# Kernel tuning notes

Measured on AMD Instinct MI355X. Metric: run time of the kernel, lower is better.

Reference implementation:

```python
import jax, jax.numpy as jnp
import numpy as np

LR = 0.1  # forward default lr; noise_std=0.0 default so no Langevin noise
B, DX, DY, H, K = 65536, 256, 64, 512, 4


def setup_inputs() -> dict:
    key = jax.random.key(0)
    ks = jax.random.split(key, 8)
    x = jax.random.normal(ks[0], (B, DX), dtype=jnp.float32)
    t = jax.random.randint(ks[1], (B,), 0, K, dtype=jnp.int64)
    # MLP params, Kaiming-ish scaling
    s1 = 1.0 / np.sqrt(DX + DY)
    s2 = 1.0 / np.sqrt(H)
    W1 = jax.random.normal(ks[2], (DX + DY, H), dtype=jnp.float32) * s1
    b1 = jnp.zeros((H,), jnp.float32)
    W2 = jax.random.normal(ks[3], (H, H), dtype=jnp.float32) * s2
    b2 = jnp.zeros((H,), jnp.float32)
    W3 = jax.random.normal(ks[4], (H, K), dtype=jnp.float32) * s2
    b3 = jnp.zeros((K,), jnp.float32)
    return {"x": x, "t": t, "W1": W1, "b1": b1, "W2": W2, "b2": b2,
            "W3": W3, "b3": b3, "steps": 20}


def reference(x, t, W1, b1, W2, b2, W3, b3, steps):
    # gather index: t.clamp_min(0) -> [B, 1]
    tc = jnp.clip(t, 0, None).astype(jnp.int32)[:, None]
    d_y = W1.shape[0] - x.shape[1]

    def energy_sum(y):
        h = jax.nn.relu(jnp.concatenate([x, y], axis=-1) @ W1 + b1)
        h = jax.nn.relu(h @ W2 + b2)
        e = h @ W3 + b3                      # [B, K]
        return jnp.take_along_axis(e, tc, axis=1).sum()

    grad_e = jax.grad(energy_sum)

    def step(y, _):
        return y - LR * grad_e(y), None

    y0 = jnp.zeros((x.shape[0], d_y), dtype=x.dtype)
    y_final, _ = jax.lax.scan(step, y0, None, length=steps)
    return y_final
```

## Files before the change

### kernel.cpp

```cpp
#include <hip/hip_runtime.h>

typedef _Float16 f16x8 __attribute__((ext_vector_type(8)));
typedef float f32x4 __attribute__((ext_vector_type(4)));

#define HID   512
#define DXD   256
#define DYD   64
#define NROWS 64
#define NTHR  1024
#define LRC   0.1f
#define TAU1  1e-4f
#define TAU2  1e-4f
#define SC12  2.44140625e-4f

#define OFF_W1YB 0
#define OFF_W1Y4 32768
#define OFF_W2B  65536
#define OFF_W2B3 327680
#define PH       589824
#define RB       1179648
#define OFF_RW1YB 0
#define OFF_RW2B  32768
#define RPA      294912
#define NCONV    884736

#define L_H0  0
#define L_H1  65536
#define HPL   65536
#define L_Y0  131072
#define L_Y1  139264
#define YPL   8192
#define L_TL  147456
#define SMEM_BYTES 147712

__device__ __forceinline__ void f2h2(float v, unsigned short* ph, unsigned short* pm) {
    unsigned short hb, mb;
    if (fabsf(v) >= 6.103515625e-05f) {
        _Float16 h = (_Float16)v;
        _Float16 m = (_Float16)((v - (float)h) * 4096.0f);
        hb = __builtin_bit_cast(unsigned short, h);
        mb = __builtin_bit_cast(unsigned short, m);
    } else {
        _Float16 m = (_Float16)(v * 4096.0f);
        hb = 0;
        mb = __builtin_bit_cast(unsigned short, m);
    }
    *ph = hb; *pm = mb;
}

template<int KSTEPS, int SROWA, int APL_>
__device__ __forceinline__ void gemmh1(const char* ldsA, const unsigned short* Bfrag,
                                       int l4, int l16, int lane, int ct,
                                       f32x4 acc[4], f32x4 accm[4])
{
    const int cb0 = l4 * 16;
    #pragma unroll
    for (int kk = 0; kk < KSTEPS; ++kk) {
        const int cb = kk * 64 + cb0;
        f16x8 ah[4], am[4];
        #pragma unroll
        for (int mt = 0; mt < 4; ++mt) {
            const int row = mt * 16 + l16;
            const int off = row * SROWA + (cb ^ ((row & 7) << 4));
            ah[mt] = *(const f16x8*)(ldsA + off);
            am[mt] = *(const f16x8*)(ldsA + APL_ + off);
        }
        const size_t boff = ((size_t)(ct * KSTEPS + kk) * 64 + lane) * 16;
        f16x8 bh = *(const f16x8*)((const char*)Bfrag + boff);
        f16x8 bm = *(const f16x8*)((const char*)(Bfrag + PH) + boff);
        #pragma unroll
        for (int mt = 0; mt < 4; ++mt) {
            acc[mt]  = __builtin_amdgcn_mfma_f32_16x16x32_f16(ah[mt], bh, acc[mt],  0, 0, 0);
            accm[mt] = __builtin_amdgcn_mfma_f32_16x16x32_f16(ah[mt], bm, accm[mt], 0, 0, 0);
            accm[mt] = __builtin_amdgcn_mfma_f32_16x16x32_f16(am[mt], bh, accm[mt], 0, 0, 0);
        }
    }
}

__device__ __attribute__((noinline))
float rescue_s2(const char* smem, int row, int col, float b2n,
                const unsigned short* __restrict__ wsb) {
    float r = b2n;
    const int xr = (row & 7) << 4;
    const int rb = row * 1024;
    const char* wh = (const char*)(wsb + RB + OFF_RW2B) + (size_t)col * 1024;
    const char* wm = (const char*)(wsb + RB + RPA + OFF_RW2B) + (size_t)col * 1024;
    for (int j0 = 0; j0 < HID; j0 += 8) {
        const int off = rb + ((j0 * 2) ^ xr);
        f16x8 h  = *(const f16x8*)(smem + L_H0 + off);
        f16x8 m_ = *(const f16x8*)(smem + L_H1 + off);
        f16x8 bh = *(const f16x8*)(wh + j0 * 2);
        f16x8 bm = *(const f16x8*)(wm + j0 * 2);
        #pragma unroll
        for (int u = 0; u < 8; ++u) {
            float hv = (float)h[u]  + (float)m_[u] * SC12;
            float wv = (float)bh[u] + (float)bm[u] * SC12;
            r = fmaf(hv, wv, r);
        }
    }
    return r;
}

__device__ __attribute__((noinline))
float rescue_s1(const char* smem, int row, int col, float cval,
                const unsigned short* __restrict__ wsb) {
    float r = cval;
    const int xr = (row & 7) << 4;
    const int rb = row * 128;
    const char* wh = (const char*)(wsb + RB + OFF_RW1YB) + (size_t)col * 128;
    const char* wm = (const char*)(wsb + RB + RPA + OFF_RW1YB) + (size_t)col * 128;
    for (int j0 = 0; j0 < DYD; j0 += 8) {
        const int off = rb + ((j0 * 2) ^ xr);
        f16x8 h  = *(const f16x8*)(smem + L_Y0 + off);
        f16x8 m_ = *(const f16x8*)(smem + L_Y1 + off);
        f16x8 bh = *(const f16x8*)(wh + j0 * 2);
        f16x8 bm = *(const f16x8*)(wm + j0 * 2);
        #pragma unroll
        for (int u = 0; u < 8; ++u) {
            float yv = (float)h[u]  + (float)m_[u] * SC12;
            float wv = (float)bh[u] + (float)bm[u] * SC12;
            r = fmaf(yv, wv, r);
        }
    }
    return r;
}

__global__ void wconv(const float* __restrict__ W1, const float* __restrict__ W2,
                      unsigned short* __restrict__ wsb)
{
    int i = blockIdx.x * blockDim.x + threadIdx.x;
    if (i >= NCONV) return;
    if (i < PH) {
        int il, KK, region;
        if (i < OFF_W1Y4)      { il = i;            KK = 2;  region = 0; }
        else if (i < OFF_W2B)  { il = i - OFF_W1Y4; KK = 16; region = 1; }
        else if (i < OFF_W2B3) { il = i - OFF_W2B;  KK = 16; region = 2; }
        else                   { il = i - OFF_W2B3; KK = 16; region = 3; }
        const int e    = il & 7;
        const int lane = (il >> 3) & 63;
        const int l16  = lane & 15;
        const int l4   = lane >> 4;
        const int rest = il >> 9;
        const int kk   = rest % KK;
        const int t    = rest / KK;
        const int n    = t * 16 + l16;
        const int k    = kk * 32 + l4 * 8 + e;
        float v;
        if (region == 0)      v = W1[(size_t)(256 + k) * 512 + n];
        else if (region == 1) v = W1[(size_t)(256 + n) * 512 + k];
        else if (region == 2) v = W2[(size_t)k * 512 + n];
        else                  v = W2[(size_t)n * 512 + k];
        f2h2(v, &wsb[i], &wsb[i + PH]);
    } else {
        int j = i - PH;
        float v;
        if (j < OFF_RW2B) { int n = j >> 6, k = j & 63;  v = W1[(size_t)(256 + k) * 512 + n]; }
        else { int jl = j - OFF_RW2B; int n = jl >> 9, k = jl & 511; v = W2[(size_t)k * 512 + n]; }
        f2h2(v, &wsb[RB + j], &wsb[RB + RPA + j]);
    }
}

__global__ __attribute__((amdgpu_flat_work_group_size(NTHR, NTHR), amdgpu_waves_per_eu(4, 4)))
void ebm_mfma(const float* __restrict__ x, const int* __restrict__ tt,
              const float* __restrict__ W1, const float* __restrict__ b1,
              const float* __restrict__ W2, const float* __restrict__ b2,
              const float* __restrict__ W3, const int* __restrict__ stepsp,
              const unsigned short* __restrict__ wsb, float* __restrict__ out)
{
    __shared__ __align__(16) char smem[SMEM_BYTES];

    const int tid  = threadIdx.x;
    const int w    = tid >> 6, lane = tid & 63;
    const int l4   = lane >> 4, l16 = lane & 15;
    const int r0   = blockIdx.x * NROWS;
    const int nt0  = w * 2;
    const int nsteps = *stepsp;

    if (tid < NROWS) {
        int tv = tt[r0 + tid];
        ((int*)(smem + L_TL))[tid] = tv < 0 ? 0 : tv;
    }
    for (int i = tid; i < 2 * YPL / 4; i += NTHR) ((unsigned*)(smem + L_Y0))[i] = 0u;

    {
        const float4* xg = (const float4*)(x + (size_t)r0 * DXD);
        #pragma unroll
        for (int j = 0; j < 4; ++j) {
            int i4 = j * NTHR + tid;
            ((float4*)(smem + L_H0))[i4] = xg[i4];
        }
    }
    __syncthreads();

    f32x4 c_reg[4][2];
    {
        float bb[2];
        #pragma unroll
        for (int nq = 0; nq < 2; ++nq) bb[nq] = b1[(nt0 + nq) * 16 + l16];
        #pragma unroll
        for (int mt = 0; mt < 4; ++mt)
            #pragma unroll
            for (int nq = 0; nq < 2; ++nq)
                c_reg[mt][nq] = (f32x4){bb[nq], bb[nq], bb[nq], bb[nq]};
        for (int i = 0; i < DXD; i += 4) {
            float wv[4][2];
            #pragma unroll
            for (int d = 0; d < 4; ++d)
                #pragma unroll
                for (int nq = 0; nq < 2; ++nq)
                    wv[d][nq] = W1[(size_t)(i + d) * HID + (nt0 + nq) * 16 + l16];
            #pragma unroll
            for (int mt = 0; mt < 4; ++mt)
                #pragma unroll
                for (int q = 0; q < 4; ++q) {
                    const int row = mt * 16 + l4 * 4 + q;
                    float4 xv = *(const float4*)(smem + L_H0 + row * 1024 + i * 4);
                    #pragma unroll
                    for (int nq = 0; nq < 2; ++nq) {
                        c_reg[mt][nq][q] = fmaf(xv.x, wv[0][nq], c_reg[mt][nq][q]);
                        c_reg[mt][nq][q] = fmaf(xv.y, wv[1][nq], c_reg[mt][nq][q]);
                        c_reg[mt][nq][q] = fmaf(xv.z, wv[2][nq], c_reg[mt][nq][q]);
                        c_reg[mt][nq][q] = fmaf(xv.w, wv[3][nq], c_reg[mt][nq][q]);
                    }
                }
        }
    }

    float b2v[2];
    #pragma unroll
    for (int nq = 0; nq < 2; ++nq) b2v[nq] = b2[(nt0 + nq) * 16 + l16];

    const int mt4 = w >> 2;
    const int nt4 = w & 3;
    f32x4 ym = (f32x4){0.f, 0.f, 0.f, 0.f};

    for (int s = 0; s < nsteps; ++s) {
        __syncthreads();

        unsigned mk = 0u;
        #pragma unroll
        for (int nq = 0; nq < 2; ++nq) {
            f32x4 acc[4], accm[4];
            #pragma unroll
            for (int mt = 0; mt < 4; ++mt) { acc[mt] = c_reg[mt][nq]; accm[mt] = (f32x4){0.f,0.f,0.f,0.f}; }
            gemmh1<2, 128, YPL>(smem + L_Y0, wsb + OFF_W1YB, l4, l16, lane, nt0 + nq, acc, accm);
            const int col = (nt0 + nq) * 16 + l16;
            unsigned tie = 0u;
            #pragma unroll
            for (int mt = 0; mt < 4; ++mt) {
                #pragma unroll
                for (int q = 0; q < 4; ++q) {
                    const int row = mt * 16 + l4 * 4 + q;
                    float v = acc[mt][q] + accm[mt][q] * SC12;
                    if (fabsf(v) < TAU1) tie |= 1u << (mt * 4 + q);
                    const int off = row * 1024 + ((col * 2) ^ ((row & 7) << 4));
                    if (v > 0.f) {
                        mk |= 1u << ((mt * 2 + nq) * 4 + q);
                        f2h2(v, (unsigned short*)(smem + L_H0 + off), (unsigned short*)(smem + L_H1 + off));
                    } else {
                        *(unsigned short*)(smem + L_H0 + off) = 0;
                        *(unsigned short*)(smem + L_H1 + off) = 0;
                    }
                }
            }
            if (__builtin_expect(tie != 0u, 0)) {
                #pragma unroll
                for (int mt = 0; mt < 4; ++mt) {
                    #pragma unroll
                    for (int q = 0; q < 4; ++q) {
                        if ((tie >> (mt * 4 + q)) & 1u) {
                            const int row = mt * 16 + l4 * 4 + q;
                            const float vr = rescue_s1(smem, row, col, c_reg[mt][nq][q], wsb);
                            const int off = row * 1024 + ((col * 2) ^ ((row & 7) << 4));
                            const unsigned bit = 1u << ((mt * 2 + nq) * 4 + q);
                            if (vr > 0.f) {
                                mk |= bit;
                                f2h2(vr, (unsigned short*)(smem + L_H0 + off), (unsigned short*)(smem + L_H1 + off));
                            } else {
                                mk &= ~bit;
                                *(unsigned short*)(smem + L_H0 + off) = 0;
                                *(unsigned short*)(smem + L_H1 + off) = 0;
                            }
                        }
                    }
                }
            }
            __builtin_amdgcn_sched_barrier(0);
        }
        __syncthreads();

        unsigned pos2 = 0u;
        #pragma unroll
        for (int nq = 0; nq < 2; ++nq) {
            f32x4 acc[4], accm[4];
            #pragma unroll
            for (int mt = 0; mt < 4; ++mt) { acc[mt] = (f32x4){b2v[nq],b2v[nq],b2v[nq],b2v[nq]}; accm[mt] = (f32x4){0.f,0.f,0.f,0.f}; }
            gemmh1<16, 1024, HPL>(smem + L_H0, wsb + OFF_W2B, l4, l16, lane, nt0 + nq, acc, accm);
            const int col = (nt0 + nq) * 16 + l16;
            unsigned tie = 0u;
            #pragma unroll
            for (int mt = 0; mt < 4; ++mt) {
                #pragma unroll
                for (int q = 0; q < 4; ++q) {
                    float v = acc[mt][q] + accm[mt][q] * SC12;
                    if (fabsf(v) < TAU2) tie |= 1u << (mt * 4 + q);
                    if (v > 0.f) pos2 |= 1u << ((mt * 2 + nq) * 4 + q);
                }
            }
            if (__builtin_expect(tie != 0u, 0)) {
                #pragma unroll
                for (int mt = 0; mt < 4; ++mt) {
                    #pragma unroll
                    for (int q = 0; q < 4; ++q) {
                        if ((tie >> (mt * 4 + q)) & 1u) {
                            const int row = mt * 16 + l4 * 4 + q;
                            const float vr = rescue_s2(smem, row, col, b2v[nq], wsb);
                            const unsigned bit = 1u << ((mt * 2 + nq) * 4 + q);
                            if (vr > 0.f) pos2 |= bit; else pos2 &= ~bit;
                        }
                    }
                }
            }
            __builtin_amdgcn_sched_barrier(0);
        }
        __syncthreads();

        #pragma unroll
        for (int mt = 0; mt < 4; ++mt) {
            #pragma unroll
            for (int nq = 0; nq < 2; ++nq) {
                const int col = (nt0 + nq) * 16 + l16;
                #pragma unroll
                for (int q = 0; q < 4; ++q) {
                    const int row = mt * 16 + l4 * 4 + q;
                    const int tv = ((const int*)(smem + L_TL))[row];
                    const int off = row * 1024 + ((col * 2) ^ ((row & 7) << 4));
                    if ((pos2 >> ((mt * 2 + nq) * 4 + q)) & 1u) {
                        f2h2(W3[col * 4 + tv],
                             (unsigned short*)(smem + L_H0 + off),
                             (unsigned short*)(smem + L_H1 + off));
                    } else {
                        *(unsigned short*)(smem + L_H0 + off) = 0;
                        *(unsigned short*)(smem + L_H1 + off) = 0;
                    }
                }
            }
        }
        __syncthreads();

        f32x4 g2vA[4], g2vB[4];
        {
            f32x4 acc[4], accm[4];
            #pragma unroll
            for (int mt = 0; mt < 4; ++mt) { acc[mt] = (f32x4){0.f,0.f,0.f,0.f}; accm[mt] = (f32x4){0.f,0.f,0.f,0.f}; }
            gemmh1<16, 1024, HPL>(smem + L_H0, wsb + OFF_W2B3, l4, l16, lane, nt0 + 0, acc, accm);
            #pragma unroll
            for (int mt = 0; mt < 4; ++mt)
                #pragma unroll
                for (int q = 0; q < 4; ++q)
                    g2vA[mt][q] = acc[mt][q] + accm[mt][q] * SC12;
        }
        __builtin_amdgcn_sched_barrier(0);
        {
            f32x4 acc[4], accm[4];
            #pragma unroll
            for (int mt = 0; mt < 4; ++mt) { acc[mt] = (f32x4){0.f,0.f,0.f,0.f}; accm[mt] = (f32x4){0.f,0.f,0.f,0.f}; }
            gemmh1<16, 1024, HPL>(smem + L_H0, wsb + OFF_W2B3, l4, l16, lane, nt0 + 1, acc, accm);
            #pragma unroll
            for (int mt = 0; mt < 4; ++mt)
                #pragma unroll
                for (int q = 0; q < 4; ++q)
                    g2vB[mt][q] = acc[mt][q] + accm[mt][q] * SC12;
        }
        __syncthreads();

        #pragma unroll
        for (int mt = 0; mt < 4; ++mt) {
            {
                const int col2 = ((nt0 + 0) * 16 + l16) * 2;
                #pragma unroll
                for (int q = 0; q < 4; ++q) {
                    const int row = mt * 16 + l4 * 4 + q;
                    const int off = row * 1024 + (col2 ^ ((row & 7) << 4));
                    if ((mk >> ((mt * 2 + 0) * 4 + q)) & 1u) {
                        f2h2(g2vA[mt][q],
                             (unsigned short*)(smem + L_H0 + off),
                             (unsigned short*)(smem + L_H1 + off));
                    } else {
                        *(unsigned short*)(smem + L_H0 + off) = 0;
                        *(unsigned short*)(smem + L_H1 + off) = 0;
                    }
                }
            }
            {
                const int col2 = ((nt0 + 1) * 16 + l16) * 2;
                #pragma unroll
                for (int q = 0; q < 4; ++q) {
                    const int row = mt * 16 + l4 * 4 + q;
                    const int off = row * 1024 + (col2 ^ ((row & 7) << 4));
                    if ((mk >> ((mt * 2 + 1) * 4 + q)) & 1u) {
                        f2h2(g2vB[mt][q],
                             (unsigned short*)(smem + L_H0 + off),
                             (unsigned short*)(smem + L_H1 + off));
                    } else {
                        *(unsigned short*)(smem + L_H0 + off) = 0;
                        *(unsigned short*)(smem + L_H1 + off) = 0;
                    }
                }
            }
        }
        __syncthreads();

        f32x4 gA = (f32x4){0.f, 0.f, 0.f, 0.f}, gAm = gA;
        {
            const char* bh0 = (const char*)(wsb + OFF_W1Y4);
            const char* bm0 = (const char*)(wsb + PH + OFF_W1Y4);
            #pragma unroll
            for (int kk = 0; kk < 16; ++kk) {
                const int cb = kk * 64 + l4 * 16;
                const int row = mt4 * 16 + l16;
                const int offA = row * 1024 + (cb ^ ((row & 7) << 4));
                f16x8 ah = *(const f16x8*)(smem + L_H0 + offA);
                f16x8 am = *(const f16x8*)(smem + L_H1 + offA);
                const size_t boff = ((size_t)(nt4 * 16 + kk) * 64 + lane) * 16;
                f16x8 bAh = *(const f16x8*)(bh0 + boff);
                f16x8 bAm = *(const f16x8*)(bm0 + boff);
                gA  = __builtin_amdgcn_mfma_f32_16x16x32_f16(ah, bAh, gA,  0, 0, 0);
                gAm = __builtin_amdgcn_mfma_f32_16x16x32_f16(ah, bAm, gAm, 0, 0, 0);
                gAm = __builtin_amdgcn_mfma_f32_16x16x32_f16(am, bAh, gAm, 0, 0, 0);
            }
        }
        #pragma unroll
        for (int q = 0; q < 4; ++q)
            ym[q] = ym[q] - LRC * (gA[q] + gAm[q] * SC12);
        #pragma unroll
        for (int q = 0; q < 4; ++q) {
            const int row = mt4 * 16 + l4 * 4 + q;
            const int col = nt4 * 16 + l16;
            const int off = row * 128 + ((col * 2) ^ ((row & 7) << 4));
            f2h2(ym[q], (unsigned short*)(smem + L_Y0 + off),
                        (unsigned short*)(smem + L_Y1 + off));
        }
    }

    #pragma unroll
    for (int q = 0; q < 4; ++q) {
        const int row = mt4 * 16 + l4 * 4 + q;
        const int col = nt4 * 16 + l16;
        out[(size_t)(r0 + row) * DYD + col] = ym[q];
    }
}

extern "C" void kernel_launch(void* const* d_in, const int* in_sizes, int n_in,
                              void* d_out, int out_size, void* d_ws, size_t ws_size,
                              hipStream_t stream) {
    const float* x  = (const float*)d_in[0];
    const int*   t  = (const int*)d_in[1];
    const float* W1 = (const float*)d_in[2];
    const float* b1 = (const float*)d_in[3];
    const float* W2 = (const float*)d_in[4];
    const float* b2 = (const float*)d_in[5];
    const float* W3 = (const float*)d_in[6];
    const int* steps = (const int*)d_in[8];
    float* out = (float*)d_out;
    unsigned short* wsb = (unsigned short*)d_ws;

    const int B = in_sizes[0] / DXD;
    const int nblocks = B / NROWS;

    wconv<<<(NCONV + 255) / 256, 256, 0, stream>>>(W1, W2, wsb);

    ebm_mfma<<<nblocks, NTHR, 0, stream>>>(x, t, W1, b1, W2, b2, W3, steps, wsb, out);
}
```

Before: 26.87 ms.

## Halve block to 8 waves, each computing four column tiles

The block size drops from 16 to 8 waves. Each wave now covers four 16-column tiles instead of two in every GEMM phase, and two output tiles in the final y-gradient GEMM. The launch bounds change to allow two blocks per CU. The aim is to reuse A-fragment loads from LDS across more MFMAs and lower barrier cost, at the price of more registers per thread (c_reg doubles to 4x4, g2v grows), which could reduce occupancy or cause spills.

```diff
diff --git a/kernel.cpp b/kernel.cpp
--- a/kernel.cpp
+++ b/kernel.cpp
@@ -7,7 +7,7 @@
 #define DXD   256
 #define DYD   64
 #define NROWS 64
-#define NTHR  1024
+#define NTHR  512
 #define LRC   0.1f
 #define TAU1  1e-4f
 #define TAU2  1e-4f
@@ -160,7 +160,7 @@
     }
 }
 
-__global__ __attribute__((amdgpu_flat_work_group_size(NTHR, NTHR), amdgpu_waves_per_eu(4, 4)))
+__global__ __launch_bounds__(NTHR, 2)
 void ebm_mfma(const float* __restrict__ x, const int* __restrict__ tt,
               const float* __restrict__ W1, const float* __restrict__ b1,
               const float* __restrict__ W2, const float* __restrict__ b2,
@@ -173,7 +173,7 @@
     const int w    = tid >> 6, lane = tid & 63;
     const int l4   = lane >> 4, l16 = lane & 15;
     const int r0   = blockIdx.x * NROWS;
-    const int nt0  = w * 2;
+    const int nt0  = w * 4;
     const int nsteps = *stepsp;
 
     if (tid < NROWS) {
@@ -185,29 +185,29 @@
     {
         const float4* xg = (const float4*)(x + (size_t)r0 * DXD);
         #pragma unroll
-        for (int j = 0; j < 4; ++j) {
+        for (int j = 0; j < 8; ++j) {
             int i4 = j * NTHR + tid;
             ((float4*)(smem + L_H0))[i4] = xg[i4];
         }
     }
     __syncthreads();
 
-    f32x4 c_reg[4][2];
+    f32x4 c_reg[4][4];
     {
-        float bb[2];
-        #pragma unroll
-        for (int nq = 0; nq < 2; ++nq) bb[nq] = b1[(nt0 + nq) * 16 + l16];
+        float bb[4];
+        #pragma unroll
+        for (int nq = 0; nq < 4; ++nq) bb[nq] = b1[(nt0 + nq) * 16 + l16];
         #pragma unroll
         for (int mt = 0; mt < 4; ++mt)
             #pragma unroll
-            for (int nq = 0; nq < 2; ++nq)
+            for (int nq = 0; nq < 4; ++nq)
                 c_reg[mt][nq] = (f32x4){bb[nq], bb[nq], bb[nq], bb[nq]};
         for (int i = 0; i < DXD; i += 4) {
-            float wv[4][2];
+            float wv[4][4];
             #pragma unroll
             for (int d = 0; d < 4; ++d)
                 #pragma unroll
-                for (int nq = 0; nq < 2; ++nq)
+                for (int nq = 0; nq < 4; ++nq)
                     wv[d][nq] = W1[(size_t)(i + d) * HID + (nt0 + nq) * 16 + l16];
             #pragma unroll
             for (int mt = 0; mt < 4; ++mt)
@@ -216,7 +216,7 @@
                     const int row = mt * 16 + l4 * 4 + q;
                     float4 xv = *(const float4*)(smem + L_H0 + row * 1024 + i * 4);
                     #pragma unroll
-                    for (int nq = 0; nq < 2; ++nq) {
+                    for (int nq = 0; nq < 4; ++nq) {
                         c_reg[mt][nq][q] = fmaf(xv.x, wv[0][nq], c_reg[mt][nq][q]);
                         c_reg[mt][nq][q] = fmaf(xv.y, wv[1][nq], c_reg[mt][nq][q]);
                         c_reg[mt][nq][q] = fmaf(xv.z, wv[2][nq], c_reg[mt][nq][q]);
@@ -226,20 +226,22 @@
         }
     }
 
-    float b2v[2];
+    float b2v[4];
     #pragma unroll
-    for (int nq = 0; nq < 2; ++nq) b2v[nq] = b2[(nt0 + nq) * 16 + l16];
-
-    const int mt4 = w >> 2;
-    const int nt4 = w & 3;
-    f32x4 ym = (f32x4){0.f, 0.f, 0.f, 0.f};
+    for (int nq = 0; nq < 4; ++nq) b2v[nq] = b2[(nt0 + nq) * 16 + l16];
+
+    const int mt4 = w >> 1;
+    const int ntA = (w & 1) * 2;
+    const int ntB = ntA + 1;
+    f32x4 ymA = (f32x4){0.f, 0.f, 0.f, 0.f};
+    f32x4 ymB = (f32x4){0.f, 0.f, 0.f, 0.f};
 
     for (int s = 0; s < nsteps; ++s) {
         __syncthreads();
 
-        unsigned mk = 0u;
-        #pragma unroll
-        for (int nq = 0; nq < 2; ++nq) {
+        unsigned long long mk = 0ull;
+        #pragma unroll
+        for (int nq = 0; nq < 4; ++nq) {
             f32x4 acc[4], accm[4];
             #pragma unroll
             for (int mt = 0; mt < 4; ++mt) { acc[mt] = c_reg[mt][nq]; accm[mt] = (f32x4){0.f,0.f,0.f,0.f}; }
@@ -255,7 +257,7 @@
                     if (fabsf(v) < TAU1) tie |= 1u << (mt * 4 + q);
                     const int off = row * 1024 + ((col * 2) ^ ((row & 7) << 4));
                     if (v > 0.f) {
-                        mk |= 1u << ((mt * 2 + nq) * 4 + q);
+                        mk |= 1ull << ((mt * 4 + nq) * 4 + q);
                         f2h2(v, (unsigned short*)(smem + L_H0 + off), (unsigned short*)(smem + L_H1 + off));
                     } else {
                         *(unsigned short*)(smem + L_H0 + off) = 0;
@@ -272,7 +274,7 @@
                             const int row = mt * 16 + l4 * 4 + q;
                             const float vr = rescue_s1(smem, row, col, c_reg[mt][nq][q], wsb);
                             const int off = row * 1024 + ((col * 2) ^ ((row & 7) << 4));
-                            const unsigned bit = 1u << ((mt * 2 + nq) * 4 + q);
+                            const unsigned long long bit = 1ull << ((mt * 4 + nq) * 4 + q);
                             if (vr > 0.f) {
                                 mk |= bit;
                                 f2h2(vr, (unsigned short*)(smem + L_H0 + off), (unsigned short*)(smem + L_H1 + off));
@@ -289,9 +291,9 @@
         }
         __syncthreads();
 
-        unsigned pos2 = 0u;
-        #pragma unroll
-        for (int nq = 0; nq < 2; ++nq) {
+        unsigned long long pos2 = 0ull;
+        #pragma unroll
+        for (int nq = 0; nq < 4; ++nq) {
             f32x4 acc[4], accm[4];
             #pragma unroll
             for (int mt = 0; mt < 4; ++mt) { acc[mt] = (f32x4){b2v[nq],b2v[nq],b2v[nq],b2v[nq]}; accm[mt] = (f32x4){0.f,0.f,0.f,0.f}; }
@@ -304,7 +306,7 @@
                 for (int q = 0; q < 4; ++q) {
                     float v = acc[mt][q] + accm[mt][q] * SC12;
                     if (fabsf(v) < TAU2) tie |= 1u << (mt * 4 + q);
-                    if (v > 0.f) pos2 |= 1u << ((mt * 2 + nq) * 4 + q);
+                    if (v > 0.f) pos2 |= 1ull << ((mt * 4 + nq) * 4 + q);
                 }
             }
             if (__builtin_expect(tie != 0u, 0)) {
@@ -315,7 +317,7 @@
                         if ((tie >> (mt * 4 + q)) & 1u) {
                             const int row = mt * 16 + l4 * 4 + q;
                             const float vr = rescue_s2(smem, row, col, b2v[nq], wsb);
-                            const unsigned bit = 1u << ((mt * 2 + nq) * 4 + q);
+                            const unsigned long long bit = 1ull << ((mt * 4 + nq) * 4 + q);
                             if (vr > 0.f) pos2 |= bit; else pos2 &= ~bit;
                         }
                     }
@@ -328,14 +330,14 @@
         #pragma unroll
         for (int mt = 0; mt < 4; ++mt) {
             #pragma unroll
-            for (int nq = 0; nq < 2; ++nq) {
+            for (int nq = 0; nq < 4; ++nq) {
                 const int col = (nt0 + nq) * 16 + l16;
                 #pragma unroll
                 for (int q = 0; q < 4; ++q) {
                     const int row = mt * 16 + l4 * 4 + q;
                     const int tv = ((const int*)(smem + L_TL))[row];
                     const int off = row * 1024 + ((col * 2) ^ ((row & 7) << 4));
-                    if ((pos2 >> ((mt * 2 + nq) * 4 + q)) & 1u) {
+                    if ((pos2 >> ((mt * 4 + nq) * 4 + q)) & 1ull) {
                         f2h2(W3[col * 4 + tv],
                              (unsigned short*)(smem + L_H0 + off),
                              (unsigned short*)(smem + L_H1 + off));
@@ -348,42 +350,33 @@
         }
         __syncthreads();
 
-        f32x4 g2vA[4], g2vB[4];
-        {
+        f32x4 g2v[4][4];
+        #pragma unroll
+        for (int nq = 0; nq < 4; ++nq) {
             f32x4 acc[4], accm[4];
             #pragma unroll
             for (int mt = 0; mt < 4; ++mt) { acc[mt] = (f32x4){0.f,0.f,0.f,0.f}; accm[mt] = (f32x4){0.f,0.f,0.f,0.f}; }
-            gemmh1<16, 1024, HPL>(smem + L_H0, wsb + OFF_W2B3, l4, l16, lane, nt0 + 0, acc, accm);
+            gemmh1<16, 1024, HPL>(smem + L_H0, wsb + OFF_W2B3, l4, l16, lane, nt0 + nq, acc, accm);
             #pragma unroll
             for (int mt = 0; mt < 4; ++mt)
                 #pragma unroll
                 for (int q = 0; q < 4; ++q)
-                    g2vA[mt][q] = acc[mt][q] + accm[mt][q] * SC12;
-        }
-        __builtin_amdgcn_sched_barrier(0);
-        {
-            f32x4 acc[4], accm[4];
-            #pragma unroll
-            for (int mt = 0; mt < 4; ++mt) { acc[mt] = (f32x4){0.f,0.f,0.f,0.f}; accm[mt] = (f32x4){0.f,0.f,0.f,0.f}; }
-            gemmh1<16, 1024, HPL>(smem + L_H0, wsb + OFF_W2B3, l4, l16, lane, nt0 + 1, acc, accm);
-            #pragma unroll
-            for (int mt = 0; mt < 4; ++mt)
-                #pragma unroll
-                for (int q = 0; q < 4; ++q)
-                    g2vB[mt][q] = acc[mt][q] + accm[mt][q] * SC12;
+                    g2v[mt][nq][q] = acc[mt][q] + accm[mt][q] * SC12;
+            __builtin_amdgcn_sched_barrier(0);
         }
         __syncthreads();
 
         #pragma unroll
         for (int mt = 0; mt < 4; ++mt) {
-            {
-                const int col2 = ((nt0 + 0) * 16 + l16) * 2;
+            #pragma unroll
+            for (int nq = 0; nq < 4; ++nq) {
+                const int col2 = ((nt0 + nq) * 16 + l16) * 2;
                 #pragma unroll
                 for (int q = 0; q < 4; ++q) {
                     const int row = mt * 16 + l4 * 4 + q;
                     const int off = row * 1024 + (col2 ^ ((row & 7) << 4));
-                    if ((mk >> ((mt * 2 + 0) * 4 + q)) & 1u) {
-                        f2h2(g2vA[mt][q],
+                    if ((mk >> ((mt * 4 + nq) * 4 + q)) & 1ull) {
+                        f2h2(g2v[mt][nq][q],
                              (unsigned short*)(smem + L_H0 + off),
                              (unsigned short*)(smem + L_H1 + off));
                     } else {
@@ -392,26 +385,11 @@
                     }
                 }
             }
-            {
-                const int col2 = ((nt0 + 1) * 16 + l16) * 2;
-                #pragma unroll
-                for (int q = 0; q < 4; ++q) {
-                    const int row = mt * 16 + l4 * 4 + q;
-                    const int off = row * 1024 + (col2 ^ ((row & 7) << 4));
-                    if ((mk >> ((mt * 2 + 1) * 4 + q)) & 1u) {
-                        f2h2(g2vB[mt][q],
-                             (unsigned short*)(smem + L_H0 + off),
-                             (unsigned short*)(smem + L_H1 + off));
-                    } else {
-                        *(unsigned short*)(smem + L_H0 + off) = 0;
-                        *(unsigned short*)(smem + L_H1 + off) = 0;
-                    }
-                }
-            }
         }
         __syncthreads();
 
         f32x4 gA = (f32x4){0.f, 0.f, 0.f, 0.f}, gAm = gA;
+        f32x4 gB = gA, gBm = gA;
         {
             const char* bh0 = (const char*)(wsb + OFF_W1Y4);
             const char* bm0 = (const char*)(wsb + PH + OFF_W1Y4);
@@ -422,32 +400,50 @@
                 const int offA = row * 1024 + (cb ^ ((row & 7) << 4));
                 f16x8 ah = *(const f16x8*)(smem + L_H0 + offA);
                 f16x8 am = *(const f16x8*)(smem + L_H1 + offA);
-                const size_t boff = ((size_t)(nt4 * 16 + kk) * 64 + lane) * 16;
-                f16x8 bAh = *(const f16x8*)(bh0 + boff);
-                f16x8 bAm = *(const f16x8*)(bm0 + boff);
+                const size_t boffA = ((size_t)(ntA * 16 + kk) * 64 + lane) * 16;
+                const size_t boffB = ((size_t)(ntB * 16 + kk) * 64 + lane) * 16;
+                f16x8 bAh = *(const f16x8*)(bh0 + boffA);
+                f16x8 bAm = *(const f16x8*)(bm0 + boffA);
+                f16x8 bBh = *(const f16x8*)(bh0 + boffB);
+                f16x8 bBm = *(const f16x8*)(bm0 + boffB);
                 gA  = __builtin_amdgcn_mfma_f32_16x16x32_f16(ah, bAh, gA,  0, 0, 0);
                 gAm = __builtin_amdgcn_mfma_f32_16x16x32_f16(ah, bAm, gAm, 0, 0, 0);
                 gAm = __builtin_amdgcn_mfma_f32_16x16x32_f16(am, bAh, gAm, 0, 0, 0);
-            }
-        }
-        #pragma unroll
-        for (int q = 0; q < 4; ++q)
-            ym[q] = ym[q] - LRC * (gA[q] + gAm[q] * SC12);
+                gB  = __builtin_amdgcn_mfma_f32_16x16x32_f16(ah, bBh, gB,  0, 0, 0);
+                gBm = __builtin_amdgcn_mfma_f32_16x16x32_f16(ah, bBm, gBm, 0, 0, 0);
+                gBm = __builtin_amdgcn_mfma_f32_16x16x32_f16(am, bBh, gBm, 0, 0, 0);
+            }
+        }
+        #pragma unroll
+        for (int q = 0; q < 4; ++q) {
+            ymA[q] = ymA[q] - LRC * (gA[q] + gAm[q] * SC12);
+            ymB[q] = ymB[q] - LRC * (gB[q] + gBm[q] * SC12);
+        }
+        #pragma unroll
+        for (int tt2 = 0; tt2 < 2; ++tt2) {
+            const int nt = tt2 ? ntB : ntA;
+            const f32x4 y = tt2 ? ymB : ymA;
+            #pragma unroll
+            for (int q = 0; q < 4; ++q) {
+                const int row = mt4 * 16 + l4 * 4 + q;
+                const int col = nt * 16 + l16;
+                const int off = row * 128 + ((col * 2) ^ ((row & 7) << 4));
+                f2h2(y[q], (unsigned short*)(smem + L_Y0 + off),
+                           (unsigned short*)(smem + L_Y1 + off));
+            }
+        }
+    }
+
+    #pragma unroll
+    for (int tt2 = 0; tt2 < 2; ++tt2) {
+        const int nt = tt2 ? ntB : ntA;
+        const f32x4 y = tt2 ? ymB : ymA;
         #pragma unroll
         for (int q = 0; q < 4; ++q) {
             const int row = mt4 * 16 + l4 * 4 + q;
-            const int col = nt4 * 16 + l16;
-            const int off = row * 128 + ((col * 2) ^ ((row & 7) << 4));
-            f2h2(ym[q], (unsigned short*)(smem + L_Y0 + off),
-                        (unsigned short*)(smem + L_Y1 + off));
-        }
-    }
-
-    #pragma unroll
-    for (int q = 0; q < 4; ++q) {
-        const int row = mt4 * 16 + l4 * 4 + q;
-        const int col = nt4 * 16 + l16;
-        out[(size_t)(r0 + row) * DYD + col] = ym[q];
+            const int col = nt * 16 + l16;
+            out[(size_t)(r0 + row) * DYD + col] = y[q];
+        }
     }
 }
 
```

Result: slower. 32.75 ms (+21.9%).
